# Optimization experiments

Measured on AMD Instinct MI355X. Metric: run time of the kernel, lower is better.

The kernel has to match this reference:

```python
import jax, jax.numpy as jnp
import numpy as np


def conv1x1(x, w, b):
    # x: [B,C,H,W], w: [O,C], b: [O]  (1x1 conv == per-pixel matmul)
    return jnp.einsum('oc,bchw->bohw', w, x) + b[None, :, None, None]


def setup_inputs() -> dict:
    key = jax.random.key(0)
    ks = jax.random.split(key, 8)
    B, C, H, W = 8, 256, 64, 64
    heads, points = 8, 4
    x = jax.random.normal(ks[0], (B, C, H, W), dtype=jnp.float32)
    # small offset weights so sampling grids stay mostly in-range (original inits these to 0)
    w_off = jax.random.normal(ks[1], (heads * points * 2, C), dtype=jnp.float32) * 0.01
    b_off = jax.random.normal(ks[2], (heads * points * 2,), dtype=jnp.float32) * 0.05
    w_attn = jax.random.normal(ks[3], (heads * points, C), dtype=jnp.float32) * 0.02
    b_attn = jnp.full((heads * points,), np.log(1.0 / points), dtype=jnp.float32)
    w_val = jax.random.normal(ks[4], (C, C), dtype=jnp.float32) * (1.0 / np.sqrt(C))
    b_val = jnp.zeros((C,), dtype=jnp.float32)
    w_out = jax.random.normal(ks[5], (C, C), dtype=jnp.float32) * (1.0 / np.sqrt(C))
    b_out = jnp.zeros((C,), dtype=jnp.float32)
    return {"x": x, "w_off": w_off, "b_off": b_off, "w_attn": w_attn, "b_attn": b_attn,
            "w_val": w_val, "b_val": b_val, "w_out": w_out, "b_out": b_out,
            "num_heads": heads, "num_points": points}


def _grid_sample_one(v, g):
    # v: [Cph,H,W] value image; g: [P,H,W,2] sampling grid in [-1,1] (x,y), align_corners=True,
    # bilinear, zero padding. Returns [Cph,P,H,W].
    Cph, H, W = v.shape
    ix = (g[..., 0] + 1.0) * 0.5 * (W - 1)  # [P,H,W]
    iy = (g[..., 1] + 1.0) * 0.5 * (H - 1)
    x0 = jnp.floor(ix); y0 = jnp.floor(iy)
    x1 = x0 + 1.0;      y1 = y0 + 1.0
    wx1 = ix - x0; wx0 = 1.0 - wx1
    wy1 = iy - y0; wy0 = 1.0 - wy1

    def corner(yc, xc, w):
        valid = (xc >= 0) & (xc <= W - 1) & (yc >= 0) & (yc <= H - 1)
        yi = jnp.clip(yc, 0, H - 1).astype(jnp.int32)
        xi = jnp.clip(xc, 0, W - 1).astype(jnp.int32)
        vv = v[:, yi, xi]  # [Cph,P,H,W]
        return vv * (w * valid.astype(w.dtype))[None]

    return (corner(y0, x0, wy0 * wx0) + corner(y0, x1, wy0 * wx1)
            + corner(y1, x0, wy1 * wx0) + corner(y1, x1, wy1 * wx1))


def deformable_attention(x, w_off, b_off, w_attn, b_attn, w_val, b_val, w_out, b_out,
                         num_heads, num_points):
    B, C, H, W = x.shape
    hd, P = num_heads, num_points
    cph = C // hd

    value = conv1x1(x, w_val, b_val)                       # [B,C,H,W]
    offsets = conv1x1(x, w_off, b_off)                     # [B,hd*P*2,H,W]
    attn = conv1x1(x, w_attn, b_attn).reshape(B, hd, P, H, W)
    attn = jax.nn.softmax(attn, axis=2)                    # softmax over points

    gy = jnp.linspace(-1.0, 1.0, H, dtype=x.dtype)
    gx = jnp.linspace(-1.0, 1.0, W, dtype=x.dtype)
    base = jnp.stack(jnp.meshgrid(gx, gy, indexing='xy'), axis=-1)  # [H,W,2] (x,y)

    off = offsets.reshape(B, hd, P, 2, H, W).transpose(0, 1, 2, 4, 5, 3)  # [B,hd,P,H,W,2]
    grid = base[None, None, None] + off                                   # [B,hd,P,H,W,2]

    val = value.reshape(B * hd, cph, H, W)
    grid = grid.reshape(B * hd, P, H, W, 2)
    sampled = jax.vmap(_grid_sample_one)(val, grid)        # [B*hd,cph,P,H,W]
    sampled = sampled.reshape(B, hd, cph, P, H, W)

    weighted = (sampled * attn[:, :, None]).sum(axis=3)    # [B,hd,cph,H,W]
    weighted = weighted.reshape(B, C, H, W)
    return conv1x1(weighted, w_out, b_out) + x


def reference(x, w_off, b_off, w_attn, b_attn, w_val, b_val, w_out, b_out,
              num_heads, num_points):
    return deformable_attention(x, w_off, b_off, w_attn, b_attn, w_val, b_val,
                                w_out, b_out, num_heads, num_points)
```

## Files before the change

### kernel.cpp

```cpp
#include <hip/hip_runtime.h>
#include <cstddef>

#define HW 4096

typedef __attribute__((ext_vector_type(8))) short short8v;
typedef __attribute__((ext_vector_type(4))) float f32x4;

__device__ inline unsigned short f2bf(float f) {
    unsigned int u = __float_as_uint(f);
    u += 0x7FFFu + ((u >> 16) & 1u);
    return (unsigned short)(u >> 16);
}
__device__ inline float bf2f(unsigned short s) {
    return __uint_as_float(((unsigned int)s) << 16);
}

#define GLOAD_LDS16(gp, lp) __builtin_amdgcn_global_load_lds( \
    (const __attribute__((address_space(1))) unsigned int*)(gp), \
    (__attribute__((address_space(3))) unsigned int*)(lp), 16, 0, 0)

__device__ inline void stage_panel(const unsigned short* __restrict__ g,
                                   unsigned short* lds, int wid, int lane)
{
    const int rsub = lane >> 5;
    const int slot = lane & 31;
#pragma unroll
    for (int i = 0; i < 16; ++i) {
        const int row = wid * 32 + i * 2 + rsub;
        GLOAD_LDS16(g + row * 256 + ((slot ^ (row & 15)) << 3),
                    lds + (wid * 32 + i * 2) * 256);
    }
}

__device__ inline short8v read_frag256(const unsigned short* lds, int row, int kbyte)
{
    const char* p = (const char*)lds + row * 512 + (kbyte ^ ((row & 15) << 4));
    return *(const short8v*)p;
}

__device__ inline void compute_pass(const unsigned short* Al, const unsigned short* Bl,
                                    int wm, int wn, int mloc, int ksel, f32x4 acc[4][4])
{
#pragma unroll
    for (int kk = 0; kk < 8; ++kk) {
        const int kb = kk * 64 + ksel * 16;
        short8v a[4], bb[4];
#pragma unroll
        for (int f = 0; f < 4; ++f) a[f]  = read_frag256(Al, wm * 64 + f * 16 + mloc, kb);
#pragma unroll
        for (int f = 0; f < 4; ++f) bb[f] = read_frag256(Bl, wn * 64 + f * 16 + mloc, kb);
#pragma unroll
        for (int fm = 0; fm < 4; ++fm)
#pragma unroll
            for (int fn = 0; fn < 4; ++fn)
                acc[fm][fn] = __builtin_amdgcn_mfma_f32_16x16x32_bf16(a[fm], bb[fn], acc[fm][fn], 0, 0, 0);
    }
}

__global__ __launch_bounds__(256)
void prep_kernel(const float* __restrict__ w_off, const float* __restrict__ b_off,
                 const float* __restrict__ w_attn, const float* __restrict__ b_attn,
                 const float* __restrict__ w_val, const float* __restrict__ b_val,
                 const float* __restrict__ w_out,
                 unsigned short* __restrict__ wcat_bf, unsigned short* __restrict__ wauxlo,
                 unsigned short* __restrict__ wout_bf, float* __restrict__ bcat)
{
    int i = blockIdx.x * 256 + threadIdx.x;
    if (i < 384 * 256) {
        int n = i >> 8, k = i & 255;
        float v;
        if (n < 256)      v = w_val[n * 256 + k];
        else if (n < 320) v = w_off[(n - 256) * 256 + k];
        else if (n < 352) v = w_attn[(n - 320) * 256 + k];
        else              v = 0.0f;
        unsigned short hi = f2bf(v);
        wcat_bf[i] = hi;
        if (n >= 256) wauxlo[(n - 256) * 256 + k] = f2bf(v - bf2f(hi));
    }
    if (i < 256 * 256) wout_bf[i] = f2bf(w_out[i]);
    if (i < 512) {
        float v = 0.0f;
        if (i < 256)      v = b_val[i];
        else if (i < 320) v = b_off[i - 256];
        else if (i < 352) v = b_attn[i - 320];
        bcat[i] = v;
    }
}

__global__ __launch_bounds__(256)
void transpose_kernel(const float* __restrict__ x, unsigned short* __restrict__ xhi)
{
    __shared__ float t[64][65];
    const int bid = blockIdx.x;
    const int pt = bid & 63, ct = (bid >> 6) & 3, b = bid >> 8;
    const int tid = threadIdx.x;
    const int rr = tid >> 4, c4 = (tid & 15) * 4;

    const float* src = x + ((size_t)(b * 256 + ct * 64)) * HW + pt * 64;
#pragma unroll
    for (int j = 0; j < 4; ++j) {
        float4 v = *(const float4*)&src[(size_t)(j * 16 + rr) * HW + c4];
        t[j * 16 + rr][c4 + 0] = v.x; t[j * 16 + rr][c4 + 1] = v.y;
        t[j * 16 + rr][c4 + 2] = v.z; t[j * 16 + rr][c4 + 3] = v.w;
    }
    __syncthreads();

    const size_t obase = ((size_t)b * HW + pt * 64) * 256 + ct * 64;
#pragma unroll
    for (int j = 0; j < 4; ++j) {
        int p = j * 16 + rr;
        ushort4 hi = make_ushort4(f2bf(t[c4 + 0][p]), f2bf(t[c4 + 1][p]),
                                  f2bf(t[c4 + 2][p]), f2bf(t[c4 + 3][p]));
        *(ushort4*)&xhi[obase + (size_t)p * 256 + c4] = hi;
    }
}

__global__ __launch_bounds__(256)
void proj_kernel(const unsigned short* __restrict__ wcat_bf, const unsigned short* __restrict__ wauxlo,
                 const unsigned short* __restrict__ xhi, const float* __restrict__ bcat,
                 unsigned short* __restrict__ value_bf,
                 float* __restrict__ off_ws, float* __restrict__ attn_ws)
{
    __shared__ unsigned short smem[2 * 128 * 256];
    unsigned short* Al = smem;
    unsigned short* Bl = smem + 128 * 256;

    const int bid = blockIdx.x;
    const int pt = bid & 31;
    const int mt = (bid >> 5) % 3;
    const int b  = bid / 96;
    const int tid = threadIdx.x, wid = tid >> 6, lane = tid & 63;
    const int wm = wid >> 1, wn = wid & 1;
    const int mloc = lane & 15, ksel = lane >> 4;

    stage_panel(xhi + ((size_t)b * HW + pt * 128) * 256, Bl, wid, lane);

    f32x4 acc[4][4];
#pragma unroll
    for (int fm = 0; fm < 4; ++fm) {
        float4 bv = *(const float4*)&bcat[mt * 128 + wm * 64 + fm * 16 + ksel * 4];
#pragma unroll
        for (int fn = 0; fn < 4; ++fn) acc[fm][fn] = (f32x4){bv.x, bv.y, bv.z, bv.w};
    }

    if (mt < 2) {
        stage_panel(wcat_bf + mt * 128 * 256, Al, wid, lane);
        __syncthreads();
        compute_pass(Al, Bl, wm, wn, mloc, ksel, acc);

#pragma unroll
        for (int fm = 0; fm < 4; ++fm) {
            const int ch = mt * 128 + wm * 64 + fm * 16 + ksel * 4;
            const int head = ch >> 5, c32 = ch & 31;
#pragma unroll
            for (int fn = 0; fn < 4; ++fn) {
                const int p = pt * 128 + wn * 64 + fn * 16 + mloc;
                f32x4 v = acc[fm][fn];
                ushort4 st = make_ushort4(f2bf(v[0]), f2bf(v[1]), f2bf(v[2]), f2bf(v[3]));
                *(ushort4*)&value_bf[(((size_t)(b * 8 + head)) * HW + p) * 32 + c32] = st;
            }
        }
    } else {
        stage_panel(wcat_bf + 256 * 256, Al, wid, lane);
        __syncthreads();
        compute_pass(Al, Bl, wm, wn, mloc, ksel, acc);
        __syncthreads();
        stage_panel(wauxlo, Al, wid, lane);
        __syncthreads();
        compute_pass(Al, Bl, wm, wn, mloc, ksel, acc);

#pragma unroll
        for (int fm = 0; fm < 4; ++fm) {
            const int ch0 = wm * 64 + fm * 16 + ksel * 4;
#pragma unroll
            for (int fn = 0; fn < 4; ++fn) {
                const int p = pt * 128 + wn * 64 + fn * 16 + mloc;
                f32x4 v = acc[fm][fn];
                if (ch0 < 64) {
                    *(float4*)&off_ws[((size_t)b * HW + p) * 64 + ch0] =
                        make_float4(v[0], v[1], v[2], v[3]);
                } else if (ch0 < 96) {
                    *(float4*)&attn_ws[((size_t)b * HW + p) * 32 + (ch0 - 64)] =
                        make_float4(v[0], v[1], v[2], v[3]);
                }
            }
        }
    }
}

__global__ __launch_bounds__(256)
void sample_kernel(const unsigned short* __restrict__ value_bf, const float* __restrict__ off_ws,
                   const float* __restrict__ attn_ws, unsigned short* __restrict__ wgt_t)
{
    const int bid    = blockIdx.x;
    const int ptile  = bid & 127;
    const int head   = (bid >> 7) & 7;
    const int b      = bid >> 10;
    const int tid    = threadIdx.x;
    const int c4     = tid & 7;
    const int posIdx = tid >> 3;
    const int p      = ptile * 32 + posIdx;
    const int h      = p >> 6;
    const int w      = p & 63;

    const float gx = w * (2.0f / 63.0f) - 1.0f;
    const float gy = h * (2.0f / 63.0f) - 1.0f;

    float4 la = *(const float4*)&attn_ws[((size_t)b * HW + p) * 32 + head * 4];
    float m  = fmaxf(fmaxf(la.x, la.y), fmaxf(la.z, la.w));
    float e0 = __expf(la.x - m), e1 = __expf(la.y - m), e2 = __expf(la.z - m), e3 = __expf(la.w - m);
    float inv = 1.0f / (e0 + e1 + e2 + e3);
    float aw[4] = {e0 * inv, e1 * inv, e2 * inv, e3 * inv};

    float4 acc = make_float4(0.f, 0.f, 0.f, 0.f);
    const unsigned short* vb = value_bf + (size_t)(b * 8 + head) * HW * 32 + c4 * 4;
    const float* offp = off_ws + ((size_t)b * HW + p) * 64 + head * 8;

#pragma unroll
    for (int pt = 0; pt < 4; ++pt) {
        float ox = offp[pt * 2 + 0];
        float oy = offp[pt * 2 + 1];
        float ix = (gx + ox + 1.0f) * 31.5f;
        float iy = (gy + oy + 1.0f) * 31.5f;
        float x0f = floorf(ix), y0f = floorf(iy);
        float wx1 = ix - x0f, wx0 = 1.0f - wx1;
        float wy1 = iy - y0f, wy0 = 1.0f - wy1;
        int x0 = (int)x0f, y0 = (int)y0f;
        int x1 = x0 + 1,   y1 = y0 + 1;
        float a = aw[pt];
        float vx0 = (x0 >= 0 && x0 <= 63) ? 1.f : 0.f;
        float vx1 = (x1 >= 0 && x1 <= 63) ? 1.f : 0.f;
        float vy0 = (y0 >= 0 && y0 <= 63) ? 1.f : 0.f;
        float vy1 = (y1 >= 0 && y1 <= 63) ? 1.f : 0.f;
        float w00 = a * wy0 * wx0 * vy0 * vx0;
        float w01 = a * wy0 * wx1 * vy0 * vx1;
        float w10 = a * wy1 * wx0 * vy1 * vx0;
        float w11 = a * wy1 * wx1 * vy1 * vx1;
        int cx0 = min(max(x0, 0), 63), cx1 = min(max(x1, 0), 63);
        int cy0 = min(max(y0, 0), 63), cy1 = min(max(y1, 0), 63);
        ushort4 u00 = *(const ushort4*)&vb[(size_t)(cy0 * 64 + cx0) * 32];
        ushort4 u01 = *(const ushort4*)&vb[(size_t)(cy0 * 64 + cx1) * 32];
        ushort4 u10 = *(const ushort4*)&vb[(size_t)(cy1 * 64 + cx0) * 32];
        ushort4 u11 = *(const ushort4*)&vb[(size_t)(cy1 * 64 + cx1) * 32];
        acc.x += w00 * bf2f(u00.x) + w01 * bf2f(u01.x) + w10 * bf2f(u10.x) + w11 * bf2f(u11.x);
        acc.y += w00 * bf2f(u00.y) + w01 * bf2f(u01.y) + w10 * bf2f(u10.y) + w11 * bf2f(u11.y);
        acc.z += w00 * bf2f(u00.z) + w01 * bf2f(u01.z) + w10 * bf2f(u10.z) + w11 * bf2f(u11.z);
        acc.w += w00 * bf2f(u00.w) + w01 * bf2f(u01.w) + w10 * bf2f(u10.w) + w11 * bf2f(u11.w);
    }

    ushort4 st = make_ushort4(f2bf(acc.x), f2bf(acc.y), f2bf(acc.z), f2bf(acc.w));
    *(ushort4*)&wgt_t[((size_t)b * HW + p) * 256 + head * 32 + c4 * 4] = st;
}

#define EPW 132
__global__ __launch_bounds__(256)
void outproj_gemm(const unsigned short* __restrict__ wout_bf, const unsigned short* __restrict__ wgt_t,
                  const float* __restrict__ b_out, const float* __restrict__ x,
                  float* __restrict__ out)
{
    __shared__ unsigned short smem[2 * 128 * 256];
    unsigned short* Al = smem;
    unsigned short* Bl = smem + 128 * 256;

    const int bid = blockIdx.x;
    const int pt = bid & 31, mt = (bid >> 5) & 1, b = bid >> 6;
    const int tid = threadIdx.x, wid = tid >> 6, lane = tid & 63;
    const int wm = wid >> 1, wn = wid & 1;
    const int mloc = lane & 15, ksel = lane >> 4;

    stage_panel(wout_bf + mt * 128 * 256, Al, wid, lane);
    stage_panel(wgt_t + ((size_t)b * HW + pt * 128) * 256, Bl, wid, lane);

    f32x4 acc[4][4];
#pragma unroll
    for (int fm = 0; fm < 4; ++fm)
#pragma unroll
        for (int fn = 0; fn < 4; ++fn) acc[fm][fn] = (f32x4){0.f, 0.f, 0.f, 0.f};

    __syncthreads();
    compute_pass(Al, Bl, wm, wn, mloc, ksel, acc);
    __syncthreads();

    float* ep = (float*)smem;
#pragma unroll
    for (int fm = 0; fm < 4; ++fm) {
        const int o_loc = wm * 64 + fm * 16 + ksel * 4;
#pragma unroll
        for (int fn = 0; fn < 4; ++fn) {
            const int p_loc = wn * 64 + fn * 16 + mloc;
            f32x4 v = acc[fm][fn];
#pragma unroll
            for (int r = 0; r < 4; ++r) ep[(o_loc + r) * EPW + p_loc] = v[r];
        }
    }
    __syncthreads();

    const int p4 = (tid & 31) * 4;
    const int o0 = tid >> 5;
    const size_t gbase = ((size_t)(b * 256 + mt * 128)) * HW + pt * 128;
#pragma unroll
    for (int it = 0; it < 16; ++it) {
        const int o = o0 + it * 8;
        float bo = b_out[mt * 128 + o];
        float4 v = *(const float4*)&ep[o * EPW + p4];
        const size_t gi = gbase + (size_t)o * HW + p4;
        float4 xv = *(const float4*)&x[gi];
        *(float4*)&out[gi] = make_float4(v.x + bo + xv.x, v.y + bo + xv.y,
                                         v.z + bo + xv.z, v.w + bo + xv.w);
    }
}

extern "C" void kernel_launch(void* const* d_in, const int* in_sizes, int n_in,
                              void* d_out, int out_size, void* d_ws, size_t ws_size,
                              hipStream_t stream)
{
    const float* x      = (const float*)d_in[0];
    const float* w_off  = (const float*)d_in[1];
    const float* b_off  = (const float*)d_in[2];
    const float* w_attn = (const float*)d_in[3];
    const float* b_attn = (const float*)d_in[4];
    const float* w_val  = (const float*)d_in[5];
    const float* b_val  = (const float*)d_in[6];
    const float* w_out  = (const float*)d_in[7];
    const float* b_out  = (const float*)d_in[8];
    float* out = (float*)d_out;

    char* ws = (char*)d_ws;
    unsigned short* wcat_bf = (unsigned short*)(ws + 0);
    unsigned short* wauxlo  = (unsigned short*)(ws + 196608);
    unsigned short* wout_bf = (unsigned short*)(ws + 262144);
    float*          bcat    = (float*)(ws + 393216);
    unsigned short* xhi     = (unsigned short*)(ws + 395264);
    unsigned short* val_bf  = (unsigned short*)(ws + 17172480);
    float*          off_ws  = (float*)(ws + 33949696);
    float*          attn_ws = (float*)(ws + 42338304);
    unsigned short* wgt_t   = (unsigned short*)(ws + 46532608);

    prep_kernel<<<384, 256, 0, stream>>>(w_off, b_off, w_attn, b_attn, w_val, b_val,
                                         w_out, wcat_bf, wauxlo, wout_bf, bcat);
    transpose_kernel<<<2048, 256, 0, stream>>>(x, xhi);
    proj_kernel<<<768, 256, 0, stream>>>(wcat_bf, wauxlo, xhi, bcat, val_bf, off_ws, attn_ws);
    sample_kernel<<<8192, 256, 0, stream>>>(val_bf, off_ws, attn_ws, wgt_t);
    outproj_gemm<<<512, 256, 0, stream>>>(wout_bf, wgt_t, b_out, x, out);
}
```

Before: 80.73 us.

## Load GEMM B fragments directly from global and drop LDS epilogue staging

Both projection GEMMs stop staging the activation (B) panel in LDS and read MFMA B fragments straight from global memory. The weight panel is still staged in LDS, now through ordinary vector loads and stores with an XOR swizzle instead of global_load_lds. The output GEMM epilogue writes results plus bias and residual directly from registers instead of transposing through LDS. This halves LDS use, which may raise occupancy, but the direct global fragment reads and the strided scalar epilogue stores are less coalesced and have higher latency.

Result: slower. 92.23 us (+14.2%).

```diff
diff --git a/kernel.cpp b/kernel.cpp
--- a/kernel.cpp
+++ b/kernel.cpp
@@ -15,46 +15,22 @@
     return __uint_as_float(((unsigned int)s) << 16);
 }
 
-#define GLOAD_LDS16(gp, lp) __builtin_amdgcn_global_load_lds( \
-    (const __attribute__((address_space(1))) unsigned int*)(gp), \
-    (__attribute__((address_space(3))) unsigned int*)(lp), 16, 0, 0)
-
-__device__ inline void stage_panel(const unsigned short* __restrict__ g,
-                                   unsigned short* lds, int wid, int lane)
-{
-    const int rsub = lane >> 5;
-    const int slot = lane & 31;
+__device__ inline void stage_A(const unsigned short* __restrict__ g,
+                               unsigned short* lds, int tid)
+{
 #pragma unroll
     for (int i = 0; i < 16; ++i) {
-        const int row = wid * 32 + i * 2 + rsub;
-        GLOAD_LDS16(g + row * 256 + ((slot ^ (row & 15)) << 3),
-                    lds + (wid * 32 + i * 2) * 256);
-    }
-}
-
-__device__ inline short8v read_frag256(const unsigned short* lds, int row, int kbyte)
-{
-    const char* p = (const char*)lds + row * 512 + (kbyte ^ ((row & 15) << 4));
+        const int gi = i * 256 + tid;
+        const int r = gi >> 5, s = gi & 31;
+        short8v v = *(const short8v*)(g + gi * 8);
+        *(short8v*)((char*)lds + r * 512 + ((s ^ (r & 7)) << 4)) = v;
+    }
+}
+
+__device__ inline short8v read_fragA(const unsigned short* lds, int row, int kbyte)
+{
+    const char* p = (const char*)lds + row * 512 + (kbyte ^ ((row & 7) << 4));
     return *(const short8v*)p;
-}
-
-__device__ inline void compute_pass(const unsigned short* Al, const unsigned short* Bl,
-                                    int wm, int wn, int mloc, int ksel, f32x4 acc[4][4])
-{
-#pragma unroll
-    for (int kk = 0; kk < 8; ++kk) {
-        const int kb = kk * 64 + ksel * 16;
-        short8v a[4], bb[4];
-#pragma unroll
-        for (int f = 0; f < 4; ++f) a[f]  = read_frag256(Al, wm * 64 + f * 16 + mloc, kb);
-#pragma unroll
-        for (int f = 0; f < 4; ++f) bb[f] = read_frag256(Bl, wn * 64 + f * 16 + mloc, kb);
-#pragma unroll
-        for (int fm = 0; fm < 4; ++fm)
-#pragma unroll
-            for (int fn = 0; fn < 4; ++fn)
-                acc[fm][fn] = __builtin_amdgcn_mfma_f32_16x16x32_bf16(a[fm], bb[fn], acc[fm][fn], 0, 0, 0);
-    }
 }
 
 __global__ __launch_bounds__(256)
@@ -115,16 +91,33 @@
     }
 }
 
+__device__ inline void kloop_direct(const unsigned short* Asm, const unsigned short* __restrict__ Bg,
+                                    int wm, int mloc, int ksel, f32x4 acc[4][4])
+{
+#pragma unroll
+    for (int kk = 0; kk < 8; ++kk) {
+        const int kb = kk * 64 + ksel * 16;
+        const int ke = kk * 32 + ksel * 8;
+        short8v a[4], bbv[4];
+#pragma unroll
+        for (int f = 0; f < 4; ++f) a[f] = read_fragA(Asm, wm * 64 + f * 16 + mloc, kb);
+#pragma unroll
+        for (int f = 0; f < 4; ++f) bbv[f] = *(const short8v*)(Bg + (f * 16 + mloc) * 256 + ke);
+#pragma unroll
+        for (int fm = 0; fm < 4; ++fm)
+#pragma unroll
+            for (int fn = 0; fn < 4; ++fn)
+                acc[fm][fn] = __builtin_amdgcn_mfma_f32_16x16x32_bf16(a[fm], bbv[fn], acc[fm][fn], 0, 0, 0);
+    }
+}
+
 __global__ __launch_bounds__(256)
 void proj_kernel(const unsigned short* __restrict__ wcat_bf, const unsigned short* __restrict__ wauxlo,
                  const unsigned short* __restrict__ xhi, const float* __restrict__ bcat,
                  unsigned short* __restrict__ value_bf,
                  float* __restrict__ off_ws, float* __restrict__ attn_ws)
 {
-    __shared__ unsigned short smem[2 * 128 * 256];
-    unsigned short* Al = smem;
-    unsigned short* Bl = smem + 128 * 256;
-
+    __shared__ unsigned short Asm[128 * 256];
     const int bid = blockIdx.x;
     const int pt = bid & 31;
     const int mt = (bid >> 5) % 3;
@@ -133,7 +126,7 @@
     const int wm = wid >> 1, wn = wid & 1;
     const int mloc = lane & 15, ksel = lane >> 4;
 
-    stage_panel(xhi + ((size_t)b * HW + pt * 128) * 256, Bl, wid, lane);
+    const unsigned short* Bg = xhi + ((size_t)b * HW + pt * 128 + wn * 64) * 256;
 
     f32x4 acc[4][4];
 #pragma unroll
@@ -144,9 +137,9 @@
     }
 
     if (mt < 2) {
-        stage_panel(wcat_bf + mt * 128 * 256, Al, wid, lane);
+        stage_A(wcat_bf + mt * 128 * 256, Asm, tid);
         __syncthreads();
-        compute_pass(Al, Bl, wm, wn, mloc, ksel, acc);
+        kloop_direct(Asm, Bg, wm, mloc, ksel, acc);
 
 #pragma unroll
         for (int fm = 0; fm < 4; ++fm) {
@@ -161,13 +154,13 @@
             }
         }
     } else {
-        stage_panel(wcat_bf + 256 * 256, Al, wid, lane);
+        stage_A(wcat_bf + 256 * 256, Asm, tid);
         __syncthreads();
-        compute_pass(Al, Bl, wm, wn, mloc, ksel, acc);
+        kloop_direct(Asm, Bg, wm, mloc, ksel, acc);
         __syncthreads();
-        stage_panel(wauxlo, Al, wid, lane);
+        stage_A(wauxlo, Asm, tid);
         __syncthreads();
-        compute_pass(Al, Bl, wm, wn, mloc, ksel, acc);
+        kloop_direct(Asm, Bg, wm, mloc, ksel, acc);
 
 #pragma unroll
         for (int fm = 0; fm < 4; ++fm) {
@@ -252,24 +245,19 @@
     *(ushort4*)&wgt_t[((size_t)b * HW + p) * 256 + head * 32 + c4 * 4] = st;
 }
 
-#define EPW 132
 __global__ __launch_bounds__(256)
 void outproj_gemm(const unsigned short* __restrict__ wout_bf, const unsigned short* __restrict__ wgt_t,
                   const float* __restrict__ b_out, const float* __restrict__ x,
                   float* __restrict__ out)
 {
-    __shared__ unsigned short smem[2 * 128 * 256];
-    unsigned short* Al = smem;
-    unsigned short* Bl = smem + 128 * 256;
-
+    __shared__ unsigned short Asm[128 * 256];
     const int bid = blockIdx.x;
     const int pt = bid & 31, mt = (bid >> 5) & 1, b = bid >> 6;
     const int tid = threadIdx.x, wid = tid >> 6, lane = tid & 63;
     const int wm = wid >> 1, wn = wid & 1;
     const int mloc = lane & 15, ksel = lane >> 4;
 
-    stage_panel(wout_bf + mt * 128 * 256, Al, wid, lane);
-    stage_panel(wgt_t + ((size_t)b * HW + pt * 128) * 256, Bl, wid, lane);
+    const unsigned short* Bg = wgt_t + ((size_t)b * HW + pt * 128 + wn * 64) * 256;
 
     f32x4 acc[4][4];
 #pragma unroll
@@ -277,36 +265,24 @@
 #pragma unroll
         for (int fn = 0; fn < 4; ++fn) acc[fm][fn] = (f32x4){0.f, 0.f, 0.f, 0.f};
 
+    stage_A(wout_bf + mt * 128 * 256, Asm, tid);
     __syncthreads();
-    compute_pass(Al, Bl, wm, wn, mloc, ksel, acc);
-    __syncthreads();
-
-    float* ep = (float*)smem;
+    kloop_direct(Asm, Bg, wm, mloc, ksel, acc);
+
 #pragma unroll
     for (int fm = 0; fm < 4; ++fm) {
-        const int o_loc = wm * 64 + fm * 16 + ksel * 4;
+        const int o = mt * 128 + wm * 64 + fm * 16 + ksel * 4;
+        float4 bo = *(const float4*)&b_out[o];
 #pragma unroll
         for (int fn = 0; fn < 4; ++fn) {
-            const int p_loc = wn * 64 + fn * 16 + mloc;
+            const int p = pt * 128 + wn * 64 + fn * 16 + mloc;
+            const size_t idx = ((size_t)(b * 256 + o)) * HW + p;
             f32x4 v = acc[fm][fn];
-#pragma unroll
-            for (int r = 0; r < 4; ++r) ep[(o_loc + r) * EPW + p_loc] = v[r];
+            out[idx + 0 * HW] = v[0] + bo.x + x[idx + 0 * HW];
+            out[idx + 1 * HW] = v[1] + bo.y + x[idx + 1 * HW];
+            out[idx + 2 * HW] = v[2] + bo.z + x[idx + 2 * HW];
+            out[idx + 3 * HW] = v[3] + bo.w + x[idx + 3 * HW];
         }
-    }
-    __syncthreads();
-
-    const int p4 = (tid & 31) * 4;
-    const int o0 = tid >> 5;
-    const size_t gbase = ((size_t)(b * 256 + mt * 128)) * HW + pt * 128;
-#pragma unroll
-    for (int it = 0; it < 16; ++it) {
-        const int o = o0 + it * 8;
-        float bo = b_out[mt * 128 + o];
-        float4 v = *(const float4*)&ep[o * EPW + p4];
-        const size_t gi = gbase + (size_t)o * HW + p4;
-        float4 xv = *(const float4*)&x[gi];
-        *(float4*)&out[gi] = make_float4(v.x + bo + xv.x, v.y + bo + xv.y,
-                                         v.z + bo + xv.z, v.w + bo + xv.w);
     }
 }
 
```
